# Kernel tuning notes

Measured on AMD Instinct MI355X. Metric: run time of the kernel, lower is better.

Reference implementation:

```python
import jax, jax.numpy as jnp
import numpy as np

QC = 12          # effective quantum channels (quantum_channels//4*4)
G = 3            # number of 4-channel quantum groups
DIM = 128
NGROUPS_GN = 8
NUM_LAYER = 1

# PauliZ sign table: wire 0 is the most-significant qubit (PennyLane default.qubit)
_SIGNS = np.array([[1.0 - 2.0 * ((k >> (3 - w)) & 1) for w in range(4)]
                   for k in range(16)], dtype=np.float32)


def _apply_rx(state, phi, w):
    # state: [B,2,2,2,2] complex64; phi: [B]; RX = cos(p/2) I - i sin(p/2) X
    c = jnp.cos(0.5 * phi).astype(jnp.complex64)
    s = (-1j) * jnp.sin(0.5 * phi).astype(jnp.complex64)
    U = jnp.stack([jnp.stack([c, s], -1), jnp.stack([s, c], -1)], -2)  # [B,2,2]
    st = jnp.moveaxis(state, 1 + w, -1)
    st = jnp.einsum('bij,b...j->b...i', U, st)
    return jnp.moveaxis(st, -1, 1 + w)


def _apply_cnot(state, c, t):
    st = jnp.moveaxis(state, (1 + c, 1 + t), (-2, -1))
    st = jnp.concatenate([st[..., 0:1, :], st[..., 1:2, ::-1]], axis=-2)
    return jnp.moveaxis(st, (-2, -1), (1 + c, 1 + t))


def _circuit(x4, theta):
    # AngleEmbedding(RX) + NUM_LAYER x Basic_ansatz; x4: [B,4], theta: [4*NUM_LAYER]
    B = x4.shape[0]
    state = jnp.zeros((B, 2, 2, 2, 2), jnp.complex64).at[:, 0, 0, 0, 0].set(1.0)
    for w in range(4):
        state = _apply_rx(state, x4[:, w], w)
    for l in range(NUM_LAYER):
        th = theta[4 * l:4 * (l + 1)]
        for w in range(4):
            state = _apply_rx(state, jnp.broadcast_to(th[w], (B,)), w)
        for c in range(3):
            state = _apply_cnot(state, c, c + 1)
        state = _apply_cnot(state, 3, 0)
    probs = jnp.abs(state.reshape(B, 16)) ** 2
    return probs @ jnp.asarray(_SIGNS)  # [B,4] PauliZ expvals


def _quantum_block(x_q, qparams):
    # x_q: [B,H,W,QC]; pool spatially, run per-group circuit, broadcast back
    B, H, W, Cq = x_q.shape
    pooled = jnp.mean(x_q, axis=(1, 2)).reshape(B, Cq // 4, 4)
    y = jax.vmap(_circuit, in_axes=(1, 0), out_axes=1)(pooled, qparams)  # [B,G,4]
    y = y.reshape(B, 1, 1, Cq)
    return jnp.broadcast_to(y, (B, H, W, Cq))


def _ws_conv(x, kernel, bias):
    eps = 1e-5  # fp32 branch of WeightStandardizedConv
    mean = jnp.mean(kernel, axis=(0, 1, 2), keepdims=True)
    var = jnp.var(kernel, axis=(0, 1, 2), keepdims=True)
    k = (kernel - mean) / jnp.sqrt(var + eps)
    y = jax.lax.conv_general_dilated(x, k, (1, 1), ((1, 1), (1, 1)),
                                     dimension_numbers=('NHWC', 'HWIO', 'NHWC'))
    return y + bias


def _group_norm(x, scale, bias, groups=NGROUPS_GN, eps=1e-6):
    B, H, W, C = x.shape
    xg = x.reshape(B, H, W, groups, C // groups)
    mu = jnp.mean(xg, axis=(1, 2, 4), keepdims=True)
    var = jnp.var(xg, axis=(1, 2, 4), keepdims=True)
    xn = ((xg - mu) / jnp.sqrt(var + eps)).reshape(B, H, W, C)
    return xn * scale + bias


def setup_inputs() -> dict:
    key = jax.random.key(0)
    ks = jax.random.split(key, 8)
    B, H, W, C, T = 16, 64, 64, DIM, 512
    cc = DIM - QC  # classical conv channels = 116
    return {
        'x': jax.random.normal(ks[0], (B, H, W, C), jnp.float32),
        'time_emb': jax.random.normal(ks[1], (B, T), jnp.float32),
        'qparams': jax.random.uniform(ks[2], (G, 4), jnp.float32),
        'conv0_kernel': jax.random.normal(ks[3], (3, 3, cc, cc), jnp.float32) * 0.05,
        'conv0_bias': jnp.zeros((cc,), jnp.float32),
        'conv1_kernel': jax.random.normal(ks[4], (3, 3, cc, cc), jnp.float32) * 0.05,
        'conv1_bias': jnp.zeros((cc,), jnp.float32),
        'gn0_scale': jnp.ones((C,), jnp.float32),
        'gn0_bias': jnp.zeros((C,), jnp.float32),
        'gn1_scale': jnp.ones((C,), jnp.float32),
        'gn1_bias': jnp.zeros((C,), jnp.float32),
        'time_w': jax.random.normal(ks[5], (T, 2 * DIM), jnp.float32) * 0.02,
        'time_b': jnp.zeros((2 * DIM,), jnp.float32),
    }


def reference(x, time_emb, qparams, conv0_kernel, conv0_bias, conv1_kernel,
              conv1_bias, gn0_scale, gn0_bias, gn1_scale, gn1_bias, time_w, time_b):
    # first quantum + classical branch
    h_q = _quantum_block(x[..., :QC], qparams)
    h_c = _ws_conv(x[..., QC:], conv0_kernel, conv0_bias)
    h = jnp.concatenate([h_q, h_c], axis=-1)
    h = _group_norm(h, gn0_scale, gn0_bias)
    # FiLM conditioning from time embedding
    t = jax.nn.swish(time_emb) @ time_w + time_b  # [B, 2*DIM]
    scale, shift = jnp.split(t[:, None, None, :], 2, axis=-1)
    h = jax.nn.swish(h * (1 + scale) + shift)
    # second quantum + classical branch
    h_q2 = _quantum_block(h[..., :QC], qparams)
    h_c2 = _ws_conv(h[..., QC:], conv1_kernel, conv1_bias)
    h2 = jnp.concatenate([h_q2, h_c2], axis=-1)
    h2 = jax.nn.swish(_group_norm(h2, gn1_scale, gn1_bias))
    return x + h2
```

## Files before the change

kernel.cpp:

```cpp
#include <hip/hip_runtime.h>
#include <math.h>

#define BATCH 16
#define NPX 4096
#define CDIM 128
#define CC 116
#define KTAPS 1044

using u16 = unsigned short;
typedef __attribute__((ext_vector_type(8))) short short8;
typedef __attribute__((ext_vector_type(16))) float f32x16;

__device__ __forceinline__ float swishf(float z) {
    return z / (1.f + __expf(-z));
}
__device__ __forceinline__ float bf2f(u16 u) {
    union { unsigned int i; float f; } v; v.i = ((unsigned int)u) << 16; return v.f;
}
__device__ __forceinline__ u16 f2bf(float f) {
    union { float f; unsigned int i; } v; v.f = f;
    unsigned int r = v.i + 0x7fffu + ((v.i >> 16) & 1u);
    return (u16)(r >> 16);
}

__device__ void run_circuit(const float* ang, const float* th, float* z) {
    float ar[16], ai[16];
#pragma unroll
    for (int k = 0; k < 16; ++k) { ar[k] = 0.f; ai[k] = 0.f; }
    ar[0] = 1.f;
#pragma unroll
    for (int pass = 0; pass < 2; ++pass) {
        const float* a = pass ? th : ang;
#pragma unroll
        for (int w = 0; w < 4; ++w) {
            float half = 0.5f * a[w];
            float cth = cosf(half), sth = sinf(half);
            int m = 1 << (3 - w);
#pragma unroll
            for (int k = 0; k < 16; ++k) {
                if (k & m) continue;
                int k2 = k | m;
                float r0 = ar[k], i0 = ai[k], r1 = ar[k2], i1 = ai[k2];
                ar[k]  = cth * r0 + sth * i1;
                ai[k]  = cth * i0 - sth * r1;
                ar[k2] = sth * i0 + cth * r1;
                ai[k2] = -sth * r0 + cth * i1;
            }
        }
    }
#pragma unroll
    for (int e = 0; e < 4; ++e) {
        const int cwi[4] = {0, 1, 2, 3};
        const int twi[4] = {1, 2, 3, 0};
        int mc = 1 << (3 - cwi[e]), mt = 1 << (3 - twi[e]);
#pragma unroll
        for (int k = 0; k < 16; ++k) {
            if ((k & mc) && !(k & mt)) {
                int k2 = k | mt;
                float tr = ar[k]; ar[k] = ar[k2]; ar[k2] = tr;
                float ti = ai[k]; ai[k] = ai[k2]; ai[k2] = ti;
            }
        }
    }
    float zz[4] = {0.f, 0.f, 0.f, 0.f};
#pragma unroll
    for (int k = 0; k < 16; ++k) {
        float p = ar[k] * ar[k] + ai[k] * ai[k];
#pragma unroll
        for (int w = 0; w < 4; ++w) zz[w] += ((k >> (3 - w)) & 1) ? -p : p;
    }
#pragma unroll
    for (int w = 0; w < 4; ++w) z[w] = zz[w];
}

__global__ void k_misc(const float* __restrict__ x, float* __restrict__ part,
                       float* __restrict__ csums,
                       const float* __restrict__ te, const float* __restrict__ W,
                       const float* __restrict__ tb, float* __restrict__ t,
                       const float* __restrict__ K0, const float* __restrict__ K1,
                       u16* __restrict__ kqp0, u16* __restrict__ kqp1) {
    const int bx = blockIdx.x, tid = threadIdx.x;
    __shared__ float red[12][256];
    __shared__ float se[512];
    __shared__ float rs[256], rss[256], mb[2];
    if (bx < 128) {
        const int b = bx >> 3, seg = bx & 7;
        float s[12];
#pragma unroll
        for (int c = 0; c < 12; ++c) s[c] = 0.f;
        const float* xb = x + (size_t)(b * 4096 + seg * 512) * CDIM;
#pragma unroll
        for (int i = 0; i < 2; ++i) {
            const float4* p = (const float4*)(xb + (size_t)(tid + i * 256) * CDIM);
            float4 v0 = p[0], v1 = p[1], v2 = p[2];
            s[0] += v0.x; s[1] += v0.y; s[2] += v0.z; s[3] += v0.w;
            s[4] += v1.x; s[5] += v1.y; s[6] += v1.z; s[7] += v1.w;
            s[8] += v2.x; s[9] += v2.y; s[10] += v2.z; s[11] += v2.w;
        }
#pragma unroll
        for (int c = 0; c < 12; ++c) red[c][tid] = s[c];
        __syncthreads();
        for (int st = 128; st > 0; st >>= 1) {
            if (tid < st) {
#pragma unroll
                for (int c = 0; c < 12; ++c) red[c][tid] += red[c][tid + st];
            }
            __syncthreads();
        }
        if (tid < 12) part[bx * 12 + tid] = red[tid][0];
        return;
    }
    if (bx < 144) {
        int i = (bx - 128) * 256 + tid;
        csums[i * 2] = 0.f;
        csums[i * 2 + 1] = 0.f;
        return;
    }
    if (bx < 160) {
        const int b = bx - 144;
        for (int k = tid; k < 512; k += 256) se[k] = swishf(te[b * 512 + k]);
        __syncthreads();
        float acc = tb[tid];
        for (int k = 0; k < 512; ++k) acc += se[k] * W[k * 256 + tid];
        t[b * 256 + tid] = acc;
        return;
    }
    const int r = bx - 160;
    const float* K = (r >> 7) ? K1 : K0;
    u16* kqp = (r >> 7) ? kqp1 : kqp0;
    const int o = r & 127;
    float s = 0.f, ss = 0.f;
    if (o < CC) {
        for (int idx = tid; idx < KTAPS; idx += 256) {
            float v = K[(size_t)idx * CC + o];
            s += v; ss += v * v;
        }
    }
    rs[tid] = s; rss[tid] = ss;
    __syncthreads();
    for (int st = 128; st > 0; st >>= 1) {
        if (tid < st) { rs[tid] += rs[tid + st]; rss[tid] += rss[tid + st]; }
        __syncthreads();
    }
    if (tid == 0) {
        float m = rs[0] * (1.f / KTAPS);
        float var = rss[0] * (1.f / KTAPS) - m * m;
        mb[0] = m;
        mb[1] = rsqrtf(var + 1e-5f);
    }
    __syncthreads();
    float m = mb[0], inv = mb[1];
    for (int idx = tid; idx < 1152; idx += 256) {
        int tap = idx >> 7, ic = idx & 127;
        float v = 0.f;
        if (o < CC && ic < CC) v = (K[((size_t)tap * CC + ic) * CC + o] - m) * inv;
        int step = tap * 8 + (ic >> 4);
        int lane2 = ((ic >> 3) & 1) * 32 + (o & 31);
        int j = ic & 7;
        kqp[(size_t)(step * 4 + (o >> 5)) * 512 + lane2 * 8 + j] = f2bf(v);
    }
}

template <int MODE>
__launch_bounds__(512, 2)
__global__ void k_conv(const void* __restrict__ inp, const float* __restrict__ Acoef,
                       const float* __restrict__ Bcoef, const u16* __restrict__ kqp,
                       const float* __restrict__ bias, u16* __restrict__ outp,
                       float* __restrict__ csum) {
    __shared__ u16 As[32768];
    __shared__ float cfA[132], cfB[132];
    const int hb = blockIdx.x, b = blockIdx.y;
    const int hp = ((hb & 7) << 2) | (hb >> 3);
    const int h0 = hp * 2;
    const int tid = threadIdx.x, lane = tid & 63, wid = tid >> 6;
    const int wm = wid & 1, wn = wid >> 1;
    const int l31 = lane & 31;
    const int rr = tid >> 8, pp = (tid >> 2) & 63, ck = tid & 3;
    const int swz = (pp & 15) << 4;

    if (MODE == 1) {
        if (tid < 128) {
            int ckk = tid >> 5, ee = tid & 31;
            float a = 0.f, bbv = 0.f;
            if (tid < CC) {
                a = Acoef[b * 128 + 12 + tid];
                bbv = Bcoef[b * 128 + 12 + tid];
            }
            cfA[ckk * 33 + ee] = a;
            cfB[ckk * 33 + ee] = bbv;
        }
        __syncthreads();
    }

    float fv[32]; short8 sv[4];
    float fv2[32]; short8 sv2[4];

#define LOADCHUNK(r, fvv, svv, val) do { \
    const int hi_ = h0 + (r) - 1; \
    val = (hi_ >= 0 && hi_ < 64); \
    if (val) { \
        const size_t px_ = (size_t)((b * 64 + hi_) * 64 + pp); \
        if (MODE == 0) { \
            const float* sp_ = (const float*)inp + px_ * 128 + 12 + ck * 32; \
            if (ck < 3) { \
                _Pragma("unroll") for (int j = 0; j < 8; ++j) *(float4*)&fvv[j * 4] = ((const float4*)sp_)[j]; \
            } else { \
                _Pragma("unroll") for (int j = 0; j < 5; ++j) *(float4*)&fvv[j * 4] = ((const float4*)sp_)[j]; \
                _Pragma("unroll") for (int e = 20; e < 32; ++e) fvv[e] = 0.f; \
            } \
        } else { \
            const u16* sp_ = (const u16*)inp + px_ * 128 + ck * 32; \
            _Pragma("unroll") for (int k = 0; k < 4; ++k) svv[k] = ((const short8*)sp_)[k]; \
        } \
    } \
} while (0)

#define WRITECHUNK(r, fvv, svv, val) do { \
    u16 t_[32]; \
    if (val) { \
        if (MODE == 0) { \
            _Pragma("unroll") for (int e = 0; e < 32; ++e) t_[e] = f2bf(fvv[e]); \
        } else { \
            _Pragma("unroll") for (int e = 0; e < 32; ++e) { \
                int c_ = ck * 32 + e; \
                float f_ = bf2f((u16)svv[e >> 3][e & 7]); \
                float w_ = swishf(f_ * cfA[ck * 33 + e] + cfB[ck * 33 + e]); \
                t_[e] = (c_ < CC) ? f2bf(w_) : (u16)0; \
            } \
        } \
    } else { \
        _Pragma("unroll") for (int e = 0; e < 32; ++e) t_[e] = 0; \
    } \
    char* rb_ = (char*)As + ((r) * 64 + pp) * 256; \
    _Pragma("unroll") for (int k = 0; k < 4; ++k) \
        *(short8*)(rb_ + ((ck * 64 + k * 16) ^ swz)) = *(const short8*)&t_[k * 8]; \
} while (0)

    bool valA, valC;
    LOADCHUNK(rr, fv, sv, valA);
    LOADCHUNK(2 + rr, fv2, sv2, valC);
    WRITECHUNK(rr, fv, sv, valA);

    const u16* bp = kqp + (size_t)wn * 512 + (size_t)lane * 8;
    short8 breg[4];
#pragma unroll
    for (int s = 0; s < 4; ++s) breg[s] = *(const short8*)(bp + ((size_t)s << 11));

    const int kh16 = (lane >> 5) << 4;
    int coloff[2][3], colswz[2][3];
#pragma unroll
    for (int mf = 0; mf < 2; ++mf)
#pragma unroll
        for (int q = 0; q < 3; ++q) {
            int c = mf * 32 + l31 + q - 1;
            int cc = c < 0 ? 0 : (c > 63 ? 63 : c);
            coloff[mf][q] = cc << 7;
            colswz[mf][q] = (cc & 15) << 4;
        }
    const bool e0 = (l31 == 0), e1 = (l31 == 31);
    const short8 zero8 = {0, 0, 0, 0, 0, 0, 0, 0};
    const int rowb = wm * 8192;

    asm volatile("s_waitcnt lgkmcnt(0)" ::: "memory");
    __builtin_amdgcn_s_barrier();

    f32x16 acc[2];
#pragma unroll
    for (int mf = 0; mf < 2; ++mf)
#pragma unroll
        for (int r = 0; r < 16; ++r) acc[mf][r] = 0.f;

#define AREAD(dst, s) do { \
    const int tap_ = (s) >> 3, p_ = tap_ / 3, q_ = tap_ % 3; \
    const int chb_ = ((s) & 7) << 5; \
    dst[0] = *(const short8*)&As[rowb + p_ * 8192 + coloff[0][q_] + (((chb_ + kh16) ^ colswz[0][q_]) >> 1)]; \
    dst[1] = *(const short8*)&As[rowb + p_ * 8192 + coloff[1][q_] + (((chb_ + kh16) ^ colswz[1][q_]) >> 1)]; \
} while (0)

#define STEP(s, base, lim) do { \
    const int cur_ = ((s) - (base)) & 1, nxt_ = cur_ ^ 1; \
    if ((s) + 1 < (lim)) AREAD(afr[nxt_], (s) + 1); \
    const int q_ = ((s) >> 3) % 3; \
    short8 a0_ = afr[cur_][0], a1_ = afr[cur_][1]; \
    if (q_ == 0) a0_ = e0 ? zero8 : a0_; \
    if (q_ == 2) a1_ = e1 ? zero8 : a1_; \
    acc[0] = __builtin_amdgcn_mfma_f32_32x32x16_bf16(a0_, breg[(s) & 3], acc[0], 0, 0, 0); \
    acc[1] = __builtin_amdgcn_mfma_f32_32x32x16_bf16(a1_, breg[(s) & 3], acc[1], 0, 0, 0); \
    if ((s) + 4 < 72) breg[(s) & 3] = *(const short8*)(bp + ((size_t)((s) + 4) << 11)); \
} while (0)

    short8 afr[2][2];
    AREAD(afr[0], 0);
#pragma unroll
    for (int s = 0; s < 24; ++s) STEP(s, 0, 24);

    WRITECHUNK(2 + rr, fv2, sv2, valC);
    asm volatile("s_waitcnt lgkmcnt(0)" ::: "memory");
    __builtin_amdgcn_s_barrier();

    AREAD(afr[0], 24);
#pragma unroll
    for (int s = 24; s < 72; ++s) STEP(s, 24, 72);

    const int oc = wn * 32 + l31;
    const float bv = (oc < CC) ? bias[oc] : 0.f;
    float cs = 0.f, cq = 0.f;
    const int rbase = (lane >> 5) << 2;

    asm volatile("s_waitcnt lgkmcnt(0)" ::: "memory");
    __builtin_amdgcn_s_barrier();
#pragma unroll
    for (int mf = 0; mf < 2; ++mf) {
#pragma unroll
        for (int r = 0; r < 16; ++r) {
            int drow = (r & 3) + ((r >> 2) << 3) + rbase;
            int flat = wm * 64 + mf * 32 + drow;
            float v = acc[mf][r] + bv;
            As[flat * 128 + oc] = f2bf(v);
            cs += v;
            cq += v * v;
        }
    }
    asm volatile("s_waitcnt lgkmcnt(0)" ::: "memory");
    __builtin_amdgcn_s_barrier();
    {
        size_t obase = (size_t)(b * 4096 + h0 * 64) * 128;
#pragma unroll
        for (int k = 0; k < 4; ++k)
            *(short8*)&outp[obase + k * 4096 + tid * 8] = *(const short8*)&As[k * 4096 + tid * 8];
    }
    cs += __shfl_xor(cs, 32);
    cq += __shfl_xor(cq, 32);
    if (lane < 32) {
        atomicAdd(&csum[(b * 128 + oc) * 2], cs);
        atomicAdd(&csum[(b * 128 + oc) * 2 + 1], cq);
    }
#undef LOADCHUNK
#undef WRITECHUNK
#undef AREAD
#undef STEP
}

__global__ void k_mid0(const float* __restrict__ part, const float* __restrict__ csum,
                       const float* __restrict__ t, const float* __restrict__ gs,
                       const float* __restrict__ gb, const float* __restrict__ qp,
                       float* __restrict__ A, float* __restrict__ Bc,
                       float* __restrict__ y2) {
    __shared__ float pooled_s[192], y1s[192], sst[128][2];
    int tid = threadIdx.x;
    if (tid < 192) {
        int b = tid / 12, c = tid % 12;
        float s = 0.f;
#pragma unroll
        for (int k = 0; k < 8; ++k) s += part[(b * 8 + k) * 12 + c];
        pooled_s[tid] = s * (1.f / 4096.f);
    }
    __syncthreads();
    if (tid < 48) {
        int b = tid / 3, g = tid % 3;
        float z[4];
        run_circuit(&pooled_s[b * 12 + g * 4], qp + g * 4, z);
#pragma unroll
        for (int w = 0; w < 4; ++w) y1s[b * 12 + g * 4 + w] = z[w];
    }
    __syncthreads();
    if (tid < 128) {
        int b = tid >> 3, g = tid & 7;
        float S = 0.f, SS = 0.f;
#pragma unroll
        for (int e = 0; e < 16; ++e) {
            int orig = g * 16 + e;
            if (orig >= 12) {
                int cc = orig - 12;
                S += csum[(b * 128 + cc) * 2];
                SS += csum[(b * 128 + cc) * 2 + 1];
            }
        }
        if (g == 0) {
#pragma unroll
            for (int c = 0; c < 12; ++c) {
                float v = y1s[b * 12 + c];
                S += 4096.f * v;
                SS += 4096.f * v * v;
            }
        }
        float mu = S * (1.f / 65536.f);
        float var = SS * (1.f / 65536.f) - mu * mu;
        sst[tid][0] = mu;
        sst[tid][1] = rsqrtf(var + 1e-6f);
    }
    __syncthreads();
    for (int i = tid; i < 2048; i += 256) {
        int b = i >> 7, c = i & 127, g = c >> 4;
        float mu = sst[b * 8 + g][0], isd = sst[b * 8 + g][1];
        float sc = t[b * 256 + c], sh = t[b * 256 + 128 + c];
        float a = isd * gs[c];
        float bb = gb[c] - mu * a;
        A[i] = a * (1.f + sc);
        Bc[i] = bb * (1.f + sc) + sh;
    }
    if (tid < 48) {
        int b = tid / 3, gq = tid % 3;
        float pin[4], z[4];
        float mu = sst[b * 8][0], isd = sst[b * 8][1];
#pragma unroll
        for (int w = 0; w < 4; ++w) {
            int c = gq * 4 + w;
            float a = isd * gs[c];
            float bb = gb[c] - mu * a;
            float sc = t[b * 256 + c], sh = t[b * 256 + 128 + c];
            float v = y1s[b * 12 + c];
            pin[w] = swishf(v * (a * (1.f + sc)) + (bb * (1.f + sc) + sh));
        }
        run_circuit(pin, qp + gq * 4, z);
#pragma unroll
        for (int w = 0; w < 4; ++w) y2[b * 12 + gq * 4 + w] = z[w];
    }
}

__global__ void k_mid1(const float* __restrict__ csum, const float* __restrict__ y2,
                       const float* __restrict__ gs, const float* __restrict__ gb,
                       float* __restrict__ A2, float* __restrict__ B2,
                       float* __restrict__ oq) {
    __shared__ float sst[128][2];
    int tid = threadIdx.x;
    if (tid < 128) {
        int b = tid >> 3, g = tid & 7;
        float S = 0.f, SS = 0.f;
#pragma unroll
        for (int e = 0; e < 16; ++e) {
            int orig = g * 16 + e;
            if (orig >= 12) {
                int cc = orig - 12;
                S += csum[(b * 128 + cc) * 2];
                SS += csum[(b * 128 + cc) * 2 + 1];
            }
        }
        if (g == 0) {
#pragma unroll
            for (int c = 0; c < 12; ++c) {
                float v = y2[b * 12 + c];
                S += 4096.f * v;
                SS += 4096.f * v * v;
            }
        }
        float mu = S * (1.f / 65536.f);
        float var = SS * (1.f / 65536.f) - mu * mu;
        sst[tid][0] = mu;
        sst[tid][1] = rsqrtf(var + 1e-6f);
    }
    __syncthreads();
    for (int i = tid; i < 2048; i += 256) {
        int b = i >> 7, c = i & 127, g = c >> 4;
        float mu = sst[b * 8 + g][0], isd = sst[b * 8 + g][1];
        float a = isd * gs[c];
        A2[i] = a;
        B2[i] = gb[c] - mu * a;
    }
    if (tid < 192) {
        int b = tid / 12, c = tid % 12;
        float mu = sst[b * 8][0], isd = sst[b * 8][1];
        float a = isd * gs[c];
        float bb = gb[c] - mu * a;
        oq[b * 12 + c] = swishf(y2[b * 12 + c] * a + bb);
    }
}

__global__ void k_final(const float* __restrict__ x, const u16* __restrict__ co,
                        const float* __restrict__ A2, const float* __restrict__ B2,
                        const float* __restrict__ oq, float* __restrict__ outp) {
    const int t = blockIdx.x, b = blockIdx.y;
    const int seg = t >> 6, hraw = t & 63;
    const int h = ((hraw & 7) << 3) | (hraw >> 3);
    const int tid = threadIdx.x;
    const size_t px = (size_t)(b * 64 + h) * 64 + seg * 8 + (tid >> 5);
    const int c4 = tid & 31, c = c4 * 4;
    float4 xv = *(const float4*)(x + px * CDIM + c);
    float4 r;
    if (c4 < 3) {
        const float* q = oq + b * 12 + c;
        r.x = xv.x + q[0]; r.y = xv.y + q[1]; r.z = xv.z + q[2]; r.w = xv.w + q[3];
    } else {
        int cc = c - 12;
        const u16* hp = co + px * 128 + cc;
        float4 a = *(const float4*)(A2 + b * 128 + c);
        float4 bb = *(const float4*)(B2 + b * 128 + c);
        r.x = xv.x + swishf(bf2f(hp[0]) * a.x + bb.x);
        r.y = xv.y + swishf(bf2f(hp[1]) * a.y + bb.y);
        r.z = xv.z + swishf(bf2f(hp[2]) * a.z + bb.z);
        r.w = xv.w + swishf(bf2f(hp[3]) * a.w + bb.w);
    }
    *(float4*)(outp + px * CDIM + c) = r;
}

extern "C" void kernel_launch(void* const* d_in, const int* in_sizes, int n_in,
                              void* d_out, int out_size, void* d_ws, size_t ws_size,
                              hipStream_t stream) {
    const float* x        = (const float*)d_in[0];
    const float* time_emb = (const float*)d_in[1];
    const float* qparams  = (const float*)d_in[2];
    const float* c0k      = (const float*)d_in[3];
    const float* c0b      = (const float*)d_in[4];
    const float* c1k      = (const float*)d_in[5];
    const float* c1b      = (const float*)d_in[6];
    const float* g0s      = (const float*)d_in[7];
    const float* g0b      = (const float*)d_in[8];
    const float* g1s      = (const float*)d_in[9];
    const float* g1b      = (const float*)d_in[10];
    const float* tw       = (const float*)d_in[11];
    const float* tb       = (const float*)d_in[12];
    float* outp = (float*)d_out;
    float* ws = (float*)d_ws;

    size_t o = 0;
    auto alloc = [&](size_t n) { size_t r = o; o += (n + 15) & ~(size_t)15; return r; };
    float* part   = ws + alloc(1536);
    float* csums  = ws + alloc(8192);
    float* csum0  = csums;
    float* csum1  = csums + 4096;
    float* t      = ws + alloc(4096);
    float* A      = ws + alloc(2048);
    float* Bc     = ws + alloc(2048);
    float* A2     = ws + alloc(2048);
    float* B2     = ws + alloc(2048);
    float* y2     = ws + alloc(192);
    float* oq     = ws + alloc(192);
    u16* kqp0     = (u16*)(ws + alloc(73728));
    u16* kqp1     = (u16*)(ws + alloc(73728));
    u16* convA    = (u16*)(ws + alloc(4194304));
    u16* convB    = (u16*)(ws + alloc(4194304));

    k_misc<<<416, 256, 0, stream>>>(x, part, csums, time_emb, tw, tb, t,
                                    c0k, c1k, kqp0, kqp1);

    dim3 cgrid(32, 16);
    k_conv<0><<<cgrid, 512, 0, stream>>>(x, nullptr, nullptr, kqp0, c0b, convA, csum0);
    k_mid0<<<1, 256, 0, stream>>>(part, csum0, t, g0s, g0b, qparams, A, Bc, y2);

    k_conv<1><<<cgrid, 512, 0, stream>>>(convA, A, Bc, kqp1, c1b, convB, csum1);
    k_mid1<<<1, 256, 0, stream>>>(csum1, y2, g1s, g1b, A2, B2, oq);
    k_final<<<dim3(512, 16), 256, 0, stream>>>(x, convB, A2, B2, oq, outp);
}
```

Measured before the change: 116.0 us.

## Fuse mid-stage GroupNorm/quantum prologue into second conv kernel, drop k_mid0 launch

Removes the single-block k_mid0 kernel and has every block of the second conv recompute its batch's pooled quantum circuit, GroupNorm stats and FiLM coefficients in a prologue, overlapped with the initial global loads. Block hb==0 also writes the second quantum input's circuit output. This removes one serial tiny launch and its global round-trip. In exchange each block does redundant serial circuit work before the GEMM. The change also raises wave priority around the MFMA pairs and reorders the first-conv chunk loads and writes.

```diff
diff --git a/kernel.cpp b/kernel.cpp
--- a/kernel.cpp
+++ b/kernel.cpp
@@ -163,12 +163,16 @@
 
 template <int MODE>
 __launch_bounds__(512, 2)
-__global__ void k_conv(const void* __restrict__ inp, const float* __restrict__ Acoef,
-                       const float* __restrict__ Bcoef, const u16* __restrict__ kqp,
+__global__ void k_conv(const void* __restrict__ inp, const u16* __restrict__ kqp,
                        const float* __restrict__ bias, u16* __restrict__ outp,
-                       float* __restrict__ csum) {
+                       float* __restrict__ csum,
+                       const float* __restrict__ part, const float* __restrict__ csin,
+                       const float* __restrict__ t, const float* __restrict__ gs,
+                       const float* __restrict__ gb, const float* __restrict__ qp,
+                       float* __restrict__ y2out) {
     __shared__ u16 As[32768];
     __shared__ float cfA[132], cfB[132];
+    __shared__ float pr_pool[12], pr_y1[12], pr_pin[12], pr_sst[8][2];
     const int hb = blockIdx.x, b = blockIdx.y;
     const int hp = ((hb & 7) << 2) | (hb >> 3);
     const int h0 = hp * 2;
@@ -177,20 +181,6 @@
     const int l31 = lane & 31;
     const int rr = tid >> 8, pp = (tid >> 2) & 63, ck = tid & 3;
     const int swz = (pp & 15) << 4;
-
-    if (MODE == 1) {
-        if (tid < 128) {
-            int ckk = tid >> 5, ee = tid & 31;
-            float a = 0.f, bbv = 0.f;
-            if (tid < CC) {
-                a = Acoef[b * 128 + 12 + tid];
-                bbv = Bcoef[b * 128 + 12 + tid];
-            }
-            cfA[ckk * 33 + ee] = a;
-            cfB[ckk * 33 + ee] = bbv;
-        }
-        __syncthreads();
-    }
 
     float fv[32]; short8 sv[4];
     float fv2[32]; short8 sv2[4];
@@ -237,9 +227,79 @@
 } while (0)
 
     bool valA, valC;
-    LOADCHUNK(rr, fv, sv, valA);
-    LOADCHUNK(2 + rr, fv2, sv2, valC);
-    WRITECHUNK(rr, fv, sv, valA);
+    if (MODE == 1) {
+        LOADCHUNK(rr, fv, sv, valA);
+        LOADCHUNK(2 + rr, fv2, sv2, valC);
+
+        if (tid < 12) {
+            float s = 0.f;
+#pragma unroll
+            for (int k = 0; k < 8; ++k) s += part[(b * 8 + k) * 12 + tid];
+            pr_pool[tid] = s * (1.f / 4096.f);
+        }
+        __syncthreads();
+        if (tid < 3) {
+            float z[4];
+            run_circuit(&pr_pool[tid * 4], qp + tid * 4, z);
+#pragma unroll
+            for (int w = 0; w < 4; ++w) pr_y1[tid * 4 + w] = z[w];
+        }
+        __syncthreads();
+        if (tid < 8) {
+            const int g = tid;
+            float S = 0.f, SS = 0.f;
+#pragma unroll
+            for (int e = 0; e < 16; ++e) {
+                int orig = g * 16 + e;
+                if (orig >= 12) {
+                    int cc = orig - 12;
+                    S += csin[(b * 128 + cc) * 2];
+                    SS += csin[(b * 128 + cc) * 2 + 1];
+                }
+            }
+            if (g == 0) {
+#pragma unroll
+                for (int c = 0; c < 12; ++c) {
+                    float v = pr_y1[c];
+                    S += 4096.f * v;
+                    SS += 4096.f * v * v;
+                }
+            }
+            float mu = S * (1.f / 65536.f);
+            float var = SS * (1.f / 65536.f) - mu * mu;
+            pr_sst[g][0] = mu;
+            pr_sst[g][1] = rsqrtf(var + 1e-6f);
+        }
+        __syncthreads();
+        if (tid < 128) {
+            const int chn = tid, g = chn >> 4;
+            float mu = pr_sst[g][0], isd = pr_sst[g][1];
+            float a = isd * gs[chn];
+            float bb = gb[chn] - mu * a;
+            float sc = t[b * 256 + chn], sh = t[b * 256 + 128 + chn];
+            float Af = a * (1.f + sc);
+            float Bf = bb * (1.f + sc) + sh;
+            if (chn >= 12) {
+                int cc = chn - 12;
+                cfA[(cc >> 5) * 33 + (cc & 31)] = Af;
+                cfB[(cc >> 5) * 33 + (cc & 31)] = Bf;
+            } else {
+                pr_pin[chn] = swishf(pr_y1[chn] * Af + Bf);
+            }
+        }
+        __syncthreads();
+        if (hb == 0 && tid < 3) {
+            float z[4];
+            run_circuit(&pr_pin[tid * 4], qp + tid * 4, z);
+#pragma unroll
+            for (int w = 0; w < 4; ++w) y2out[b * 12 + tid * 4 + w] = z[w];
+        }
+        WRITECHUNK(rr, fv, sv, valA);
+    } else {
+        LOADCHUNK(rr, fv, sv, valA);
+        WRITECHUNK(rr, fv, sv, valA);
+        LOADCHUNK(2 + rr, fv2, sv2, valC);
+    }
 
     const u16* bp = kqp + (size_t)wn * 512 + (size_t)lane * 8;
     short8 breg[4];
@@ -284,8 +344,10 @@
     short8 a0_ = afr[cur_][0], a1_ = afr[cur_][1]; \
     if (q_ == 0) a0_ = e0 ? zero8 : a0_; \
     if (q_ == 2) a1_ = e1 ? zero8 : a1_; \
+    __builtin_amdgcn_s_setprio(1); \
     acc[0] = __builtin_amdgcn_mfma_f32_32x32x16_bf16(a0_, breg[(s) & 3], acc[0], 0, 0, 0); \
     acc[1] = __builtin_amdgcn_mfma_f32_32x32x16_bf16(a1_, breg[(s) & 3], acc[1], 0, 0, 0); \
+    __builtin_amdgcn_s_setprio(0); \
     if ((s) + 4 < 72) breg[(s) & 3] = *(const short8*)(bp + ((size_t)((s) + 4) << 11)); \
 } while (0)
 
@@ -339,83 +401,6 @@
 #undef WRITECHUNK
 #undef AREAD
 #undef STEP
-}
-
-__global__ void k_mid0(const float* __restrict__ part, const float* __restrict__ csum,
-                       const float* __restrict__ t, const float* __restrict__ gs,
-                       const float* __restrict__ gb, const float* __restrict__ qp,
-                       float* __restrict__ A, float* __restrict__ Bc,
-                       float* __restrict__ y2) {
-    __shared__ float pooled_s[192], y1s[192], sst[128][2];
-    int tid = threadIdx.x;
-    if (tid < 192) {
-        int b = tid / 12, c = tid % 12;
-        float s = 0.f;
-#pragma unroll
-        for (int k = 0; k < 8; ++k) s += part[(b * 8 + k) * 12 + c];
-        pooled_s[tid] = s * (1.f / 4096.f);
-    }
-    __syncthreads();
-    if (tid < 48) {
-        int b = tid / 3, g = tid % 3;
-        float z[4];
-        run_circuit(&pooled_s[b * 12 + g * 4], qp + g * 4, z);
-#pragma unroll
-        for (int w = 0; w < 4; ++w) y1s[b * 12 + g * 4 + w] = z[w];
-    }
-    __syncthreads();
-    if (tid < 128) {
-        int b = tid >> 3, g = tid & 7;
-        float S = 0.f, SS = 0.f;
-#pragma unroll
-        for (int e = 0; e < 16; ++e) {
-            int orig = g * 16 + e;
-            if (orig >= 12) {
-                int cc = orig - 12;
-                S += csum[(b * 128 + cc) * 2];
-                SS += csum[(b * 128 + cc) * 2 + 1];
-            }
-        }
-        if (g == 0) {
-#pragma unroll
-            for (int c = 0; c < 12; ++c) {
-                float v = y1s[b * 12 + c];
-                S += 4096.f * v;
-                SS += 4096.f * v * v;
-            }
-        }
-        float mu = S * (1.f / 65536.f);
-        float var = SS * (1.f / 65536.f) - mu * mu;
-        sst[tid][0] = mu;
-        sst[tid][1] = rsqrtf(var + 1e-6f);
-    }
-    __syncthreads();
-    for (int i = tid; i < 2048; i += 256) {
-        int b = i >> 7, c = i & 127, g = c >> 4;
-        float mu = sst[b * 8 + g][0], isd = sst[b * 8 + g][1];
-        float sc = t[b * 256 + c], sh = t[b * 256 + 128 + c];
-        float a = isd * gs[c];
-        float bb = gb[c] - mu * a;
-        A[i] = a * (1.f + sc);
-        Bc[i] = bb * (1.f + sc) + sh;
-    }
-    if (tid < 48) {
-        int b = tid / 3, gq = tid % 3;
-        float pin[4], z[4];
-        float mu = sst[b * 8][0], isd = sst[b * 8][1];
-#pragma unroll
-        for (int w = 0; w < 4; ++w) {
-            int c = gq * 4 + w;
-            float a = isd * gs[c];
-            float bb = gb[c] - mu * a;
-            float sc = t[b * 256 + c], sh = t[b * 256 + 128 + c];
-            float v = y1s[b * 12 + c];
-            pin[w] = swishf(v * (a * (1.f + sc)) + (bb * (1.f + sc) + sh));
-        }
-        run_circuit(pin, qp + gq * 4, z);
-#pragma unroll
-        for (int w = 0; w < 4; ++w) y2[b * 12 + gq * 4 + w] = z[w];
-    }
 }
 
 __global__ void k_mid1(const float* __restrict__ csum, const float* __restrict__ y2,
@@ -519,8 +504,6 @@
     float* csum0  = csums;
     float* csum1  = csums + 4096;
     float* t      = ws + alloc(4096);
-    float* A      = ws + alloc(2048);
-    float* Bc     = ws + alloc(2048);
     float* A2     = ws + alloc(2048);
     float* B2     = ws + alloc(2048);
     float* y2     = ws + alloc(192);
@@ -534,10 +517,11 @@
                                     c0k, c1k, kqp0, kqp1);
 
     dim3 cgrid(32, 16);
-    k_conv<0><<<cgrid, 512, 0, stream>>>(x, nullptr, nullptr, kqp0, c0b, convA, csum0);
-    k_mid0<<<1, 256, 0, stream>>>(part, csum0, t, g0s, g0b, qparams, A, Bc, y2);
-
-    k_conv<1><<<cgrid, 512, 0, stream>>>(convA, A, Bc, kqp1, c1b, convB, csum1);
+    k_conv<0><<<cgrid, 512, 0, stream>>>(x, kqp0, c0b, convA, csum0,
+                                         nullptr, nullptr, nullptr, nullptr,
+                                         nullptr, nullptr, nullptr);
+    k_conv<1><<<cgrid, 512, 0, stream>>>(convA, kqp1, c1b, convB, csum1,
+                                         part, csum0, t, g0s, g0b, qparams, y2);
     k_mid1<<<1, 256, 0, stream>>>(csum1, y2, g1s, g1b, A2, B2, oq);
     k_final<<<dim3(512, 16), 256, 0, stream>>>(x, convB, A2, B2, oq, outp);
 }
```

New measurement: 112.3 us. 3.2% less time.
